# Kernel optimization log

Measured on AMD Instinct MI355X. Metric: run time of the kernel, lower is better.

The kernel has to match this reference:

```python
import jax, jax.numpy as jnp
import numpy as np

N = 100000   # nodes
E = 1600000  # edges (avg degree 16)
D = 128      # in_channels
C = 40       # out_channels (classes)
K = 3        # propagation hops


def setup_inputs() -> dict:
    key = jax.random.key(0)
    k1, k2, k3 = jax.random.split(key, 3)
    x = jax.random.normal(k1, (N, D), dtype=jnp.float32)
    edge_index = jax.random.randint(k2, (2, E), 0, N, dtype=jnp.int64)
    W = jax.random.normal(k3, (D, C), dtype=jnp.float32) * (1.0 / np.sqrt(D))
    b = jnp.zeros((C,), dtype=jnp.float32)
    return {"x": x, "edge_index": edge_index, "W": W, "b": b}


def reference(x, edge_index, W, b):
    n = x.shape[0]
    # gcn_norm: add self-loops, symmetric degree normalization
    loop = jnp.arange(n, dtype=edge_index.dtype)
    src = jnp.concatenate([edge_index[0], loop])  # [E+N]
    dst = jnp.concatenate([edge_index[1], loop])  # [E+N]
    deg = jax.ops.segment_sum(jnp.ones(src.shape[0], x.dtype), dst, num_segments=n)
    deg_inv_sqrt = jnp.where(deg > 0, jax.lax.rsqrt(deg), 0.0)
    norm = deg_inv_sqrt[src] * deg_inv_sqrt[dst]  # [E+N]
    for _ in range(K):
        x = jax.ops.segment_sum(x[src] * norm[:, None], dst, num_segments=n)
    logits = x @ W + b  # [N, C]
    return jax.nn.log_softmax(logits, axis=1)
```

## Files before the change

kernel.cpp:

```cpp
#include <hip/hip_runtime.h>

#define D 128
#define C 40
#define NBH 256
#define BSH 8
#define NBKT_MAX 512

typedef __attribute__((ext_vector_type(8))) short s8v;
typedef __attribute__((ext_vector_type(4))) float f4v;

__device__ __forceinline__ float bf2f(unsigned short u) {
    union { unsigned int i; float f; } v; v.i = ((unsigned int)u) << 16; return v.f;
}
__device__ __forceinline__ unsigned short f2bf(float f) {
    unsigned int x = __float_as_uint(f);
    unsigned int r = (x + 0x7FFFu + ((x >> 16) & 1u)) >> 16;
    return (unsigned short)r;
}

__global__ void hist_proj_kernel(const int* __restrict__ dst, int* __restrict__ M, int E,
                                 const float* __restrict__ x, const float* __restrict__ W,
                                 unsigned short* __restrict__ y, int n, int nbkt) {
    __shared__ int shist[NBKT_MAX];
    int bid = blockIdx.x, tid = threadIdx.x;
    int role, sub;
    if (bid < 2 * NBH) { role = bid & 1; sub = bid >> 1; }
    else { role = 0; sub = bid - NBH; }

    if (role == 1) {
        for (int t = tid; t < nbkt; t += 256) shist[t] = 0;
        __syncthreads();
        for (int e = sub * 256 + tid; e < E; e += NBH * 256)
            atomicAdd(&shist[dst[e] >> BSH], 1);
        __syncthreads();
        for (int t = tid; t < nbkt; t += 256) M[t * NBH + sub] = shist[t];
        return;
    }

    int wid = tid >> 6;
    int lane = tid & 63;
    int tile = sub * 4 + wid;
    if (tile * 16 >= n) return;
    int r = lane & 15;
    int kg = lane >> 4;

    s8v bfrag[3][4];
#pragma unroll
    for (int ct = 0; ct < 3; ++ct) {
        int col = ct * 16 + r;
#pragma unroll
        for (int ks = 0; ks < 4; ++ks) {
            s8v f;
#pragma unroll
            for (int j = 0; j < 8; ++j) {
                int k = ks * 32 + kg * 8 + j;
                float wv = (col < C) ? W[k * C + col] : 0.0f;
                f[j] = (short)f2bf(wv);
            }
            bfrag[ct][ks] = f;
        }
    }

    f4v acc0 = {0.f, 0.f, 0.f, 0.f};
    f4v acc1 = {0.f, 0.f, 0.f, 0.f};
    f4v acc2 = {0.f, 0.f, 0.f, 0.f};
    int row = tile * 16 + r;
    const float4* xrow = (const float4*)(x + (size_t)row * D);
#pragma unroll
    for (int ks = 0; ks < 4; ++ks) {
        int kb = ks * 32 + kg * 8;
        float4 u0 = xrow[kb >> 2];
        float4 u1 = xrow[(kb >> 2) + 1];
        s8v af;
        af[0] = (short)f2bf(u0.x); af[1] = (short)f2bf(u0.y);
        af[2] = (short)f2bf(u0.z); af[3] = (short)f2bf(u0.w);
        af[4] = (short)f2bf(u1.x); af[5] = (short)f2bf(u1.y);
        af[6] = (short)f2bf(u1.z); af[7] = (short)f2bf(u1.w);
        acc0 = __builtin_amdgcn_mfma_f32_16x16x32_bf16(af, bfrag[0][ks], acc0, 0, 0, 0);
        acc1 = __builtin_amdgcn_mfma_f32_16x16x32_bf16(af, bfrag[1][ks], acc1, 0, 0, 0);
        acc2 = __builtin_amdgcn_mfma_f32_16x16x32_bf16(af, bfrag[2][ks], acc2, 0, 0, 0);
    }
#pragma unroll
    for (int rg = 0; rg < 4; ++rg) {
        int orow = tile * 16 + kg * 4 + rg;
        unsigned short* yr = y + (size_t)orow * C;
        yr[r] = f2bf(acc0[rg]);
        yr[16 + r] = f2bf(acc1[rg]);
        if (r < 8) yr[32 + r] = f2bf(acc2[rg]);
    }
}

__global__ void scanM_kernel(int* __restrict__ M, int* __restrict__ btot, int nbkt) {
    __shared__ int s[NBH];
    int b = blockIdx.x, tid = threadIdx.x;
    int v = M[b * NBH + tid];
    s[tid] = v;
    __syncthreads();
    for (int off = 1; off < NBH; off <<= 1) {
        int t = (tid >= off) ? s[tid - off] : 0;
        __syncthreads();
        s[tid] += t;
        __syncthreads();
    }
    M[b * NBH + tid] = s[tid] - v;
    if (tid == NBH - 1) btot[b] = s[tid];
}

__global__ void scanB_kernel(const int* __restrict__ btot, int* __restrict__ bbase,
                             int* __restrict__ rowptr, int nbkt, int n, int E) {
    __shared__ int s[512];
    int tid = threadIdx.x;
    int v = (tid < nbkt) ? btot[tid] : 0;
    s[tid] = v;
    __syncthreads();
    for (int off = 1; off < 512; off <<= 1) {
        int t = (tid >= off) ? s[tid - off] : 0;
        __syncthreads();
        s[tid] += t;
        __syncthreads();
    }
    if (tid < nbkt) bbase[tid] = s[tid] - v;
    if (tid == 0) { bbase[nbkt] = E; rowptr[n] = E; }
}

__global__ void part_kernel(const int* __restrict__ src, const int* __restrict__ dst,
                            const int* __restrict__ M, const int* __restrict__ bbase,
                            int* __restrict__ ebuf, int E, int nbkt) {
    __shared__ int scur[NBKT_MAX];
    int blk = blockIdx.x, tid = threadIdx.x;
    for (int t = tid; t < nbkt; t += 256) scur[t] = bbase[t] + M[t * NBH + blk];
    __syncthreads();
    for (int e = blk * 256 + tid; e < E; e += NBH * 256) {
        int d = dst[e];
        int pos = atomicAdd(&scur[d >> BSH], 1);
        ebuf[pos] = src[e] | ((d & ((1 << BSH) - 1)) << 17);
    }
}

__global__ void bucket_csr_kernel(const int* __restrict__ ebuf, const int* __restrict__ bbase,
                                  int* __restrict__ rowptr, float* __restrict__ dis,
                                  int* __restrict__ srcs, unsigned short* __restrict__ y, int n) {
    __shared__ int scnt[256];
    __shared__ int s[256];
    __shared__ int sptr[256];
    __shared__ float sdis[256];
    int b = blockIdx.x, tid = threadIdx.x;
    int lo = bbase[b], hi = bbase[b + 1];
    scnt[tid] = 0;
    __syncthreads();
    for (int i = lo + tid; i < hi; i += 256)
        atomicAdd(&scnt[(ebuf[i] >> 17) & 255], 1);
    __syncthreads();
    int v = scnt[tid];
    s[tid] = v;
    __syncthreads();
    for (int off = 1; off < 256; off <<= 1) {
        int t = (tid >= off) ? s[tid - off] : 0;
        __syncthreads();
        s[tid] += t;
        __syncthreads();
    }
    int excl = s[tid] - v;
    int node = b * 256 + tid;
    float dv = rsqrtf(1.0f + (float)v);
    if (node < n) { rowptr[node] = lo + excl; dis[node] = dv; }
    sdis[tid] = dv;
    sptr[tid] = lo + excl;
    __syncthreads();
    for (int i = lo + tid; i < hi; i += 256) {
        int ev = ebuf[i];
        int pos = atomicAdd(&sptr[(ev >> 17) & 255], 1);
        srcs[pos] = ev & 0x1FFFF;
    }
    __syncthreads();
    ushort4* y4 = (ushort4*)y;
    size_t base4 = (size_t)b * 256 * 10;
    for (int idx = tid; idx < 256 * 10; idx += 256) {
        int node2 = b * 256 + idx / 10;
        if (node2 < n) {
            ushort4 u = y4[base4 + idx];
            float sc = sdis[idx / 10];
            u.x = f2bf(sc * bf2f(u.x)); u.y = f2bf(sc * bf2f(u.y));
            u.z = f2bf(sc * bf2f(u.z)); u.w = f2bf(sc * bf2f(u.w));
            y4[base4 + idx] = u;
        }
    }
}

__global__ void gatherZ_kernel(const unsigned short* __restrict__ zin,
                               unsigned short* __restrict__ zout,
                               const int* __restrict__ rowptr, const int* __restrict__ srcs,
                               const float* __restrict__ dis, int n) {
    int gtid = blockIdx.x * blockDim.x + threadIdx.x;
    int node = gtid / 10;
    int ch = gtid - node * 10;
    if (node >= n) return;
    const ushort4* zi = (const ushort4*)zin;
    ushort4 sv = zi[(size_t)node * 10 + ch];
    float ax = bf2f(sv.x), ay = bf2f(sv.y), az = bf2f(sv.z), aw = bf2f(sv.w);
    int beg = rowptr[node], end = rowptr[node + 1];
    int e = beg;
    for (; e + 4 <= end; e += 4) {
        int s0 = srcs[e + 0], s1 = srcs[e + 1], s2 = srcs[e + 2], s3 = srcs[e + 3];
        ushort4 v0 = zi[(size_t)s0 * 10 + ch];
        ushort4 v1 = zi[(size_t)s1 * 10 + ch];
        ushort4 v2 = zi[(size_t)s2 * 10 + ch];
        ushort4 v3 = zi[(size_t)s3 * 10 + ch];
        ax += bf2f(v0.x) + bf2f(v1.x) + bf2f(v2.x) + bf2f(v3.x);
        ay += bf2f(v0.y) + bf2f(v1.y) + bf2f(v2.y) + bf2f(v3.y);
        az += bf2f(v0.z) + bf2f(v1.z) + bf2f(v2.z) + bf2f(v3.z);
        aw += bf2f(v0.w) + bf2f(v1.w) + bf2f(v2.w) + bf2f(v3.w);
    }
    for (; e < end; ++e) {
        ushort4 vv = zi[(size_t)srcs[e] * 10 + ch];
        ax += bf2f(vv.x); ay += bf2f(vv.y); az += bf2f(vv.z); aw += bf2f(vv.w);
    }
    float dd = dis[node];
    float sc = dd * dd;
    ushort4 o;
    o.x = f2bf(ax * sc); o.y = f2bf(ay * sc); o.z = f2bf(az * sc); o.w = f2bf(aw * sc);
    ((ushort4*)zout)[(size_t)node * 10 + ch] = o;
}

__global__ void __launch_bounds__(320)
gatherZ_lsm_kernel(const unsigned short* __restrict__ zin, const float* __restrict__ b,
                   float* __restrict__ out, const int* __restrict__ rowptr,
                   const int* __restrict__ srcs, const float* __restrict__ dis, int n) {
    __shared__ float sY[32 * C];
    __shared__ float sb[C];
    int tid = threadIdx.x;
    if (tid < C) sb[tid] = b[tid];
    int ndb = tid / 10;
    int ch = tid - ndb * 10;
    int node = blockIdx.x * 32 + ndb;
    if (node < n) {
        const ushort4* zi = (const ushort4*)zin;
        ushort4 sv = zi[(size_t)node * 10 + ch];
        float ax = bf2f(sv.x), ay = bf2f(sv.y), az = bf2f(sv.z), aw = bf2f(sv.w);
        int beg = rowptr[node], end = rowptr[node + 1];
        int e = beg;
        for (; e + 4 <= end; e += 4) {
            int s0 = srcs[e + 0], s1 = srcs[e + 1], s2 = srcs[e + 2], s3 = srcs[e + 3];
            ushort4 v0 = zi[(size_t)s0 * 10 + ch];
            ushort4 v1 = zi[(size_t)s1 * 10 + ch];
            ushort4 v2 = zi[(size_t)s2 * 10 + ch];
            ushort4 v3 = zi[(size_t)s3 * 10 + ch];
            ax += bf2f(v0.x) + bf2f(v1.x) + bf2f(v2.x) + bf2f(v3.x);
            ay += bf2f(v0.y) + bf2f(v1.y) + bf2f(v2.y) + bf2f(v3.y);
            az += bf2f(v0.z) + bf2f(v1.z) + bf2f(v2.z) + bf2f(v3.z);
            aw += bf2f(v0.w) + bf2f(v1.w) + bf2f(v2.w) + bf2f(v3.w);
        }
        for (; e < end; ++e) {
            ushort4 vv = zi[(size_t)srcs[e] * 10 + ch];
            ax += bf2f(vv.x); ay += bf2f(vv.y); az += bf2f(vv.z); aw += bf2f(vv.w);
        }
        float dd = dis[node];
        ((float4*)sY)[tid] = make_float4(ax * dd, ay * dd, az * dd, aw * dd);
    }
    __syncthreads();
    if (tid < 256) {
        int nd = tid >> 3;
        int node2 = blockIdx.x * 32 + nd;
        if (node2 < n) {
            int cg = (tid & 7) * 5;
            float a5[5];
#pragma unroll
            for (int j = 0; j < 5; ++j) a5[j] = sY[nd * C + cg + j] + sb[cg + j];
            float m = a5[0];
#pragma unroll
            for (int j = 1; j < 5; ++j) m = fmaxf(m, a5[j]);
#pragma unroll
            for (int off = 1; off < 8; off <<= 1) m = fmaxf(m, __shfl_xor(m, off, 8));
            float ssum = 0.0f;
#pragma unroll
            for (int j = 0; j < 5; ++j) ssum += __expf(a5[j] - m);
#pragma unroll
            for (int off = 1; off < 8; off <<= 1) ssum += __shfl_xor(ssum, off, 8);
            float ls = logf(ssum) + m;
            float* o = out + (size_t)node2 * C + cg;
#pragma unroll
            for (int j = 0; j < 5; ++j) o[j] = a5[j] - ls;
        }
    }
}

extern "C" void kernel_launch(void* const* d_in, const int* in_sizes, int n_in,
                              void* d_out, int out_size, void* d_ws, size_t ws_size,
                              hipStream_t stream) {
    const float* x  = (const float*)d_in[0];
    const int*   ei = (const int*)d_in[1];
    const float* W  = (const float*)d_in[2];
    const float* b  = (const float*)d_in[3];
    float* out = (float*)d_out;

    const int N = in_sizes[0] / D;
    const int E = in_sizes[1] / 2;
    const int* src = ei;
    const int* dst = ei + E;
    const int nbkt = (N + 255) >> BSH;

    size_t npad = ((size_t)N + 256) & ~(size_t)255;
    size_t epad = ((size_t)E + 255) & ~(size_t)255;
    char* p = (char*)d_ws;
    float* dis    = (float*)p;  p += npad * 4;
    int*   rowptr = (int*)p;    p += npad * 4;
    int*   btot   = (int*)p;    p += NBKT_MAX * 4;
    int*   bbase  = (int*)p;    p += (NBKT_MAX + 1) * 4;
    int*   M      = (int*)p;    p += (size_t)NBKT_MAX * NBH * 4;
    int*   ebuf   = (int*)p;    p += epad * 4;
    int*   srcs   = (int*)p;    p += epad * 4;
    size_t ypad = (((size_t)N * C * 2) + 255) & ~(size_t)255;
    unsigned short* ybuf0 = (unsigned short*)p;  p += ypad;
    unsigned short* ybuf1 = (unsigned short*)p;

    const int TB = 256;
    int ntile = (N + 15) / 16;
    int nb_p = (ntile + 3) / 4;

    hist_proj_kernel<<<NBH + nb_p, TB, 0, stream>>>(dst, M, E, x, W, ybuf0, N, nbkt);
    scanM_kernel<<<nbkt, NBH, 0, stream>>>(M, btot, nbkt);
    scanB_kernel<<<1, 512, 0, stream>>>(btot, bbase, rowptr, nbkt, N, E);
    part_kernel<<<NBH, TB, 0, stream>>>(src, dst, M, bbase, ebuf, E, nbkt);
    bucket_csr_kernel<<<nbkt, TB, 0, stream>>>(ebuf, bbase, rowptr, dis, srcs, ybuf0, N);

    int nb_g = ((N * 10) + TB - 1) / TB;
    gatherZ_kernel<<<nb_g, TB, 0, stream>>>(ybuf0, ybuf1, rowptr, srcs, dis, N);
    gatherZ_kernel<<<nb_g, TB, 0, stream>>>(ybuf1, ybuf0, rowptr, srcs, dis, N);
    int nb_l = (N + 31) / 32;
    gatherZ_lsm_kernel<<<nb_l, 320, 0, stream>>>(ybuf0, b, out, rowptr, srcs, dis, N);
}
```

Before: 173.5 us.

## Pad node feature rows to 128 bytes and stage edge partition in LDS

Feature rows of the projected bf16 matrix are padded from 80 to 128 bytes (16 ushort4 slots, 10 used), so each gathered row aligns to cache lines. The histogram and partition kernels now give each block a contiguous chunk of edges. The partition kernel does a local per-bucket histogram and scan, sorts its chunk into LDS, and then writes runs to global memory, replacing scattered global writes with grouped ones. The cost is a larger feature buffer and roughly 50 KB of LDS per partition block, which limits occupancy.

```diff
diff --git a/kernel.cpp b/kernel.cpp
--- a/kernel.cpp
+++ b/kernel.cpp
@@ -5,6 +5,8 @@
 #define NBH 256
 #define BSH 8
 #define NBKT_MAX 512
+#define EPB 6272
+#define ZS 16
 
 typedef __attribute__((ext_vector_type(8))) short s8v;
 typedef __attribute__((ext_vector_type(4))) float f4v;
@@ -30,7 +32,10 @@
     if (role == 1) {
         for (int t = tid; t < nbkt; t += 256) shist[t] = 0;
         __syncthreads();
-        for (int e = sub * 256 + tid; e < E; e += NBH * 256)
+        int chunk = (E + NBH - 1) / NBH;
+        int base = sub * chunk;
+        int lim = min(E, base + chunk);
+        for (int e = base + tid; e < lim; e += 256)
             atomicAdd(&shist[dst[e] >> BSH], 1);
         __syncthreads();
         for (int t = tid; t < nbkt; t += 256) M[t * NBH + sub] = shist[t];
@@ -83,7 +88,7 @@
 #pragma unroll
     for (int rg = 0; rg < 4; ++rg) {
         int orow = tile * 16 + kg * 4 + rg;
-        unsigned short* yr = y + (size_t)orow * C;
+        unsigned short* yr = y + (size_t)orow * (ZS * 4);
         yr[r] = f2bf(acc0[rg]);
         yr[16 + r] = f2bf(acc1[rg]);
         if (r < 8) yr[32 + r] = f2bf(acc2[rg]);
@@ -123,18 +128,54 @@
     if (tid == 0) { bbase[nbkt] = E; rowptr[n] = E; }
 }
 
-__global__ void part_kernel(const int* __restrict__ src, const int* __restrict__ dst,
-                            const int* __restrict__ M, const int* __restrict__ bbase,
-                            int* __restrict__ ebuf, int E, int nbkt) {
-    __shared__ int scur[NBKT_MAX];
+__global__ void __launch_bounds__(256)
+part_kernel(const int* __restrict__ src, const int* __restrict__ dst,
+            const int* __restrict__ M, const int* __restrict__ bbase,
+            int* __restrict__ ebuf, int E, int nbkt) {
+    __shared__ int lhist[NBKT_MAX];
+    __shared__ int ls[NBKT_MAX];
+    __shared__ int lslot[NBKT_MAX];
+    __shared__ int sdelta[NBKT_MAX];
+    __shared__ int sVal[EPB];
+    __shared__ int sG[EPB];
     int blk = blockIdx.x, tid = threadIdx.x;
-    for (int t = tid; t < nbkt; t += 256) scur[t] = bbase[t] + M[t * NBH + blk];
-    __syncthreads();
-    for (int e = blk * 256 + tid; e < E; e += NBH * 256) {
+    int chunk = (E + NBH - 1) / NBH;
+    int base = blk * chunk;
+    int lim = min(E, base + chunk);
+    int cnt = lim - base;
+
+    for (int t = tid; t < NBKT_MAX; t += 256) lhist[t] = 0;
+    __syncthreads();
+    for (int e = base + tid; e < lim; e += 256)
+        atomicAdd(&lhist[dst[e] >> BSH], 1);
+    __syncthreads();
+    {
+        int i0 = tid, i1 = tid + 256;
+        ls[i0] = lhist[i0]; ls[i1] = lhist[i1];
+        __syncthreads();
+        for (int off = 1; off < 512; off <<= 1) {
+            int v0 = (i0 >= off) ? ls[i0 - off] : 0;
+            int v1 = (i1 >= off) ? ls[i1 - off] : 0;
+            __syncthreads();
+            ls[i0] += v0; ls[i1] += v1;
+            __syncthreads();
+        }
+    }
+    for (int t = tid; t < nbkt; t += 256) {
+        int excl = ls[t] - lhist[t];
+        lslot[t] = excl;
+        sdelta[t] = bbase[t] + M[t * NBH + blk] - excl;
+    }
+    __syncthreads();
+    for (int e = base + tid; e < lim; e += 256) {
         int d = dst[e];
-        int pos = atomicAdd(&scur[d >> BSH], 1);
-        ebuf[pos] = src[e] | ((d & ((1 << BSH) - 1)) << 17);
-    }
+        int t = d >> BSH;
+        int slot = atomicAdd(&lslot[t], 1);
+        sVal[slot] = src[e] | ((d & ((1 << BSH) - 1)) << 17);
+        sG[slot] = sdelta[t] + slot;
+    }
+    __syncthreads();
+    for (int i = tid; i < cnt; i += 256) ebuf[sG[i]] = sVal[i];
 }
 
 __global__ void bucket_csr_kernel(const int* __restrict__ ebuf, const int* __restrict__ bbase,
@@ -174,12 +215,13 @@
     }
     __syncthreads();
     ushort4* y4 = (ushort4*)y;
-    size_t base4 = (size_t)b * 256 * 10;
-    for (int idx = tid; idx < 256 * 10; idx += 256) {
-        int node2 = b * 256 + idx / 10;
-        if (node2 < n) {
+    size_t base4 = (size_t)b * 256 * ZS;
+    for (int idx = tid; idx < 256 * ZS; idx += 256) {
+        int ch = idx & (ZS - 1);
+        int node2 = b * 256 + (idx >> 4);
+        if (ch < 10 && node2 < n) {
             ushort4 u = y4[base4 + idx];
-            float sc = sdis[idx / 10];
+            float sc = sdis[idx >> 4];
             u.x = f2bf(sc * bf2f(u.x)); u.y = f2bf(sc * bf2f(u.y));
             u.z = f2bf(sc * bf2f(u.z)); u.w = f2bf(sc * bf2f(u.w));
             y4[base4 + idx] = u;
@@ -196,30 +238,30 @@
     int ch = gtid - node * 10;
     if (node >= n) return;
     const ushort4* zi = (const ushort4*)zin;
-    ushort4 sv = zi[(size_t)node * 10 + ch];
+    ushort4 sv = zi[(size_t)node * ZS + ch];
     float ax = bf2f(sv.x), ay = bf2f(sv.y), az = bf2f(sv.z), aw = bf2f(sv.w);
     int beg = rowptr[node], end = rowptr[node + 1];
     int e = beg;
     for (; e + 4 <= end; e += 4) {
         int s0 = srcs[e + 0], s1 = srcs[e + 1], s2 = srcs[e + 2], s3 = srcs[e + 3];
-        ushort4 v0 = zi[(size_t)s0 * 10 + ch];
-        ushort4 v1 = zi[(size_t)s1 * 10 + ch];
-        ushort4 v2 = zi[(size_t)s2 * 10 + ch];
-        ushort4 v3 = zi[(size_t)s3 * 10 + ch];
+        ushort4 v0 = zi[(size_t)s0 * ZS + ch];
+        ushort4 v1 = zi[(size_t)s1 * ZS + ch];
+        ushort4 v2 = zi[(size_t)s2 * ZS + ch];
+        ushort4 v3 = zi[(size_t)s3 * ZS + ch];
         ax += bf2f(v0.x) + bf2f(v1.x) + bf2f(v2.x) + bf2f(v3.x);
         ay += bf2f(v0.y) + bf2f(v1.y) + bf2f(v2.y) + bf2f(v3.y);
         az += bf2f(v0.z) + bf2f(v1.z) + bf2f(v2.z) + bf2f(v3.z);
         aw += bf2f(v0.w) + bf2f(v1.w) + bf2f(v2.w) + bf2f(v3.w);
     }
     for (; e < end; ++e) {
-        ushort4 vv = zi[(size_t)srcs[e] * 10 + ch];
+        ushort4 vv = zi[(size_t)srcs[e] * ZS + ch];
         ax += bf2f(vv.x); ay += bf2f(vv.y); az += bf2f(vv.z); aw += bf2f(vv.w);
     }
     float dd = dis[node];
     float sc = dd * dd;
     ushort4 o;
     o.x = f2bf(ax * sc); o.y = f2bf(ay * sc); o.z = f2bf(az * sc); o.w = f2bf(aw * sc);
-    ((ushort4*)zout)[(size_t)node * 10 + ch] = o;
+    ((ushort4*)zout)[(size_t)node * ZS + ch] = o;
 }
 
 __global__ void __launch_bounds__(320)
@@ -235,23 +277,23 @@
     int node = blockIdx.x * 32 + ndb;
     if (node < n) {
         const ushort4* zi = (const ushort4*)zin;
-        ushort4 sv = zi[(size_t)node * 10 + ch];
+        ushort4 sv = zi[(size_t)node * ZS + ch];
         float ax = bf2f(sv.x), ay = bf2f(sv.y), az = bf2f(sv.z), aw = bf2f(sv.w);
         int beg = rowptr[node], end = rowptr[node + 1];
         int e = beg;
         for (; e + 4 <= end; e += 4) {
             int s0 = srcs[e + 0], s1 = srcs[e + 1], s2 = srcs[e + 2], s3 = srcs[e + 3];
-            ushort4 v0 = zi[(size_t)s0 * 10 + ch];
-            ushort4 v1 = zi[(size_t)s1 * 10 + ch];
-            ushort4 v2 = zi[(size_t)s2 * 10 + ch];
-            ushort4 v3 = zi[(size_t)s3 * 10 + ch];
+            ushort4 v0 = zi[(size_t)s0 * ZS + ch];
+            ushort4 v1 = zi[(size_t)s1 * ZS + ch];
+            ushort4 v2 = zi[(size_t)s2 * ZS + ch];
+            ushort4 v3 = zi[(size_t)s3 * ZS + ch];
             ax += bf2f(v0.x) + bf2f(v1.x) + bf2f(v2.x) + bf2f(v3.x);
             ay += bf2f(v0.y) + bf2f(v1.y) + bf2f(v2.y) + bf2f(v3.y);
             az += bf2f(v0.z) + bf2f(v1.z) + bf2f(v2.z) + bf2f(v3.z);
             aw += bf2f(v0.w) + bf2f(v1.w) + bf2f(v2.w) + bf2f(v3.w);
         }
         for (; e < end; ++e) {
-            ushort4 vv = zi[(size_t)srcs[e] * 10 + ch];
+            ushort4 vv = zi[(size_t)srcs[e] * ZS + ch];
             ax += bf2f(vv.x); ay += bf2f(vv.y); az += bf2f(vv.z); aw += bf2f(vv.w);
         }
         float dd = dis[node];
@@ -309,23 +351,23 @@
     int*   M      = (int*)p;    p += (size_t)NBKT_MAX * NBH * 4;
     int*   ebuf   = (int*)p;    p += epad * 4;
     int*   srcs   = (int*)p;    p += epad * 4;
-    size_t ypad = (((size_t)N * C * 2) + 255) & ~(size_t)255;
-    unsigned short* ybuf0 = (unsigned short*)p;  p += ypad;
-    unsigned short* ybuf1 = (unsigned short*)p;
+    size_t zpad = (((size_t)N * ZS * 8) + 255) & ~(size_t)255;
+    unsigned short* zbuf0 = (unsigned short*)p;  p += zpad;
+    unsigned short* zbuf1 = (unsigned short*)p;
 
     const int TB = 256;
     int ntile = (N + 15) / 16;
     int nb_p = (ntile + 3) / 4;
 
-    hist_proj_kernel<<<NBH + nb_p, TB, 0, stream>>>(dst, M, E, x, W, ybuf0, N, nbkt);
+    hist_proj_kernel<<<NBH + nb_p, TB, 0, stream>>>(dst, M, E, x, W, zbuf0, N, nbkt);
     scanM_kernel<<<nbkt, NBH, 0, stream>>>(M, btot, nbkt);
     scanB_kernel<<<1, 512, 0, stream>>>(btot, bbase, rowptr, nbkt, N, E);
     part_kernel<<<NBH, TB, 0, stream>>>(src, dst, M, bbase, ebuf, E, nbkt);
-    bucket_csr_kernel<<<nbkt, TB, 0, stream>>>(ebuf, bbase, rowptr, dis, srcs, ybuf0, N);
+    bucket_csr_kernel<<<nbkt, TB, 0, stream>>>(ebuf, bbase, rowptr, dis, srcs, zbuf0, N);
 
     int nb_g = ((N * 10) + TB - 1) / TB;
-    gatherZ_kernel<<<nb_g, TB, 0, stream>>>(ybuf0, ybuf1, rowptr, srcs, dis, N);
-    gatherZ_kernel<<<nb_g, TB, 0, stream>>>(ybuf1, ybuf0, rowptr, srcs, dis, N);
+    gatherZ_kernel<<<nb_g, TB, 0, stream>>>(zbuf0, zbuf1, rowptr, srcs, dis, N);
+    gatherZ_kernel<<<nb_g, TB, 0, stream>>>(zbuf1, zbuf0, rowptr, srcs, dis, N);
     int nb_l = (N + 31) / 32;
-    gatherZ_lsm_kernel<<<nb_l, 320, 0, stream>>>(ybuf0, b, out, rowptr, srcs, dis, N);
-}
+    gatherZ_lsm_kernel<<<nb_l, 320, 0, stream>>>(zbuf0, b, out, rowptr, srcs, dis, N);
+}
```

Measured after the change: 174.2 us. No clear change (+0.4%).
